# Optimization experiments

Measured on AMD Instinct MI355X. Metric: run time of the kernel, lower is better.

The kernel has to match this reference:

```python
import jax, jax.numpy as jnp
import numpy as np
from jax import lax

RADIUS = 4
SIGMA_1 = 5.0
SIGMA_2 = 1.0


def _gaussian_kernel_3d(radius, sigma):
    x = np.linspace(-radius, radius, 2 * radius + 1)
    xx, yy, zz = np.meshgrid(x, x, x)
    dist2 = xx ** 2 + yy ** 2 + zz ** 2
    k = np.exp(-dist2 / (2.0 * sigma ** 2)).astype(np.float32)
    return jnp.asarray(k)[None, None]  # [O=1, I=1, D, H, W]


def _conv3d_same(x, kernel, radius):
    # x: [B,1,D,H,W], kernel: [1,1,kd,kh,kw]
    pad = [(radius, radius)] * 3
    return lax.conv_general_dilated(
        x, kernel, window_strides=(1, 1, 1), padding=pad,
        dimension_numbers=('NCDHW', 'OIDHW', 'NCDHW'))


def setup_inputs() -> dict:
    key = jax.random.key(0)
    k1, k2 = jax.random.split(key)
    labels = jax.random.uniform(k1, (4, 1, 160, 160, 160), dtype=jnp.float32)
    inputs = jax.random.uniform(k2, (4, 1, 160, 160, 160), dtype=jnp.float32)
    return {"labels": labels, "inputs": inputs}


def reference(labels, inputs):
    kernel = _gaussian_kernel_3d(RADIUS, SIGMA_1)
    num_classes = 2
    p0 = labels[:, 0:1]  # [B,1,D,H,W]
    loss = jnp.float32(0.0)
    for k in range(num_classes):
        class_probs = p0 if k == 0 else 1.0 - p0
        class_mean = (jnp.mean(inputs * class_probs, axis=(2, 3, 4), keepdims=True)
                      / (jnp.mean(class_probs, axis=(2, 3, 4), keepdims=True) + 1e-5))
        diff = jnp.sum((inputs - class_mean) ** 2, axis=1, keepdims=True)  # [B,1,D,H,W]
        weights = jnp.exp(-(diff ** 2) / (SIGMA_2 ** 2))
        numerator = jnp.sum(class_probs * _conv3d_same(class_probs * weights, kernel, RADIUS))
        denominator = jnp.sum(class_probs * _conv3d_same(weights, kernel, RADIUS))
        # L1Loss(scalar, 0) == abs(scalar)
        loss = loss + jnp.abs(numerator / (denominator + 1e-6))
    return jnp.float32(num_classes) - loss
```

## Files before the change

kernel.cpp:

```cpp
#include <hip/hip_runtime.h>
#include <math.h>

#define NX   160
#define N2   25600
#define N3   4096000
#define NB   4
#define TILE 32
#define HALO 4
#define LW   40

#define NTILES_XY 16000
#define TILES_PER_B 4000
#define NBLK_Z 800

__device__ __constant__ float G1[9] = {
    0.72614903f, 0.83527021f, 0.92311635f, 0.98019867f, 1.0f,
    0.98019867f, 0.92311635f, 0.83527021f, 0.72614903f};

__device__ inline float edge_sum(int i) {
    float s = 0.f;
#pragma unroll
    for (int d = 0; d < 9; ++d) {
        int j = i + d - 4;
        s += (j >= 0 && j < NX) ? G1[d] : 0.f;
    }
    return s;
}

template <int NV>
__device__ inline void block_reduce_store(double* vals, double* dst) {
    __shared__ double red[4][NV];
    int lane = threadIdx.x & 63;
    int wave = threadIdx.x >> 6;
#pragma unroll
    for (int v = 0; v < NV; ++v) {
        double x = vals[v];
#pragma unroll
        for (int off = 32; off > 0; off >>= 1) x += __shfl_down(x, off, 64);
        if (lane == 0) red[wave][v] = x;
    }
    __syncthreads();
    if (threadIdx.x < NV) {
        int v = threadIdx.x;
        dst[v] = red[0][v] + red[1][v] + red[2][v] + red[3][v];
    }
}

__global__ __launch_bounds__(256) void conv_xy_kernel(
    const float* __restrict__ labels, const float* __restrict__ inputs,
    float* __restrict__ t, double* __restrict__ pS) {
    __shared__ float sA[LW][LW];
    __shared__ float sB[LW][TILE + 1];

    int bid = blockIdx.x;
    int tileX = bid % 5;
    int tileY = (bid / 5) % 5;
    int zb = bid / 25;
    int sliceOff = zb * N2;
    int x0 = tileX * TILE, y0 = tileY * TILE;
    int tid = threadIdx.x;

    for (int i = tid; i < LW * LW; i += 256) {
        int ly = i / LW, lx = i % LW;
        int gx = x0 + lx - HALO, gy = y0 + ly - HALO;
        float v = 0.f;
        if (gx >= 0 && gx < NX && gy >= 0 && gy < NX)
            v = labels[sliceOff + gy * NX + gx];
        sA[ly][lx] = v;
    }
    __syncthreads();

    for (int i = tid; i < LW * TILE; i += 256) {
        int ly = i / TILE, ox = i % TILE;
        float s = 0.f;
#pragma unroll
        for (int d = 0; d < 9; ++d) s += G1[d] * sA[ly][ox + d];
        sB[ly][ox] = s;
    }
    __syncthreads();

    double lp = 0.0, lip = 0.0, li = 0.0;
    for (int i = tid; i < TILE * TILE; i += 256) {
        int oy = i / TILE, ox = i % TILE;
        float s = 0.f;
#pragma unroll
        for (int d = 0; d < 9; ++d) s += G1[d] * sB[oy + d][ox];
        int gi = sliceOff + (y0 + oy) * NX + (x0 + ox);
        t[gi] = s;
        float p = sA[oy + HALO][ox + HALO];
        float in = inputs[gi];
        lp += (double)p;
        lip += (double)in * (double)p;
        li += (double)in;
    }
    double vals[3] = {lp, lip, li};
    block_reduce_store<3>(vals, pS + 3 * bid);
}

__global__ __launch_bounds__(256) void reduce_S_kernel(
    const double* __restrict__ pS, double* __restrict__ S) {
    int b = blockIdx.x;
    double v0 = 0, v1 = 0, v2 = 0;
    for (int i = threadIdx.x; i < TILES_PER_B; i += 256) {
        const double* p = pS + 3 * (b * TILES_PER_B + i);
        v0 += p[0]; v1 += p[1]; v2 += p[2];
    }
    double vals[3] = {v0, v1, v2};
    block_reduce_store<3>(vals, S + 3 * b);
}

__device__ inline float4 f4_axpy(float a, float4 b, float4 c) {
    return make_float4(c.x + a * b.x, c.y + a * b.y, c.z + a * b.z, c.w + a * b.w);
}

__global__ __launch_bounds__(256) void conv_z_reduce_kernel(
    const float* __restrict__ t, const float* __restrict__ labels,
    const float* __restrict__ inputs, const double* __restrict__ S,
    double* __restrict__ pZ) {
    int tidg = blockIdx.x * 256 + threadIdx.x;
    int x4 = tidg % 40;
    int r = tidg / 40;
    int y = r % NX;
    r /= NX;
    int zc = r % 8;
    int b = r / 8;

    double sp = S[3 * b + 0], sip = S[3 * b + 1], si = S[3 * b + 2];
    const double Nv = (double)N3;
    float m0 = (float)((sip / Nv) / (sp / Nv + 1e-5));
    float m1 = (float)(((si - sip) / Nv) / ((Nv - sp) / Nv + 1e-5));

    int x = x4 * 4;
    float ey = edge_sum(y);
    float4 Cxy = make_float4(edge_sum(x) * ey, edge_sum(x + 1) * ey,
                             edge_sum(x + 2) * ey, edge_sum(x + 3) * ey);

    int z0 = zc * 20;
    int base = b * N3 + y * NX + x;

    float4 win[9];
#pragma unroll
    for (int d = 0; d < 9; ++d) {
        int z = z0 - 4 + d;
        win[d] = (z >= 0 && z < NX) ? *(const float4*)&t[base + z * N2]
                                    : make_float4(0.f, 0.f, 0.f, 0.f);
    }

    double n0 = 0, d0 = 0, n1 = 0, d1 = 0;
    for (int z = z0; z < z0 + 20; ++z) {
        float4 c = make_float4(0.f, 0.f, 0.f, 0.f);
#pragma unroll
        for (int d = 0; d < 9; ++d) c = f4_axpy(G1[d], win[d], c);
        int gi = base + z * N2;
        float4 p = *(const float4*)&labels[gi];
        float4 in = *(const float4*)&inputs[gi];
        float ez = edge_sum(z);
        float pc[4] = {p.x, p.y, p.z, p.w};
        float ic[4] = {in.x, in.y, in.z, in.w};
        float cc[4] = {c.x, c.y, c.z, c.w};
        float cx[4] = {Cxy.x, Cxy.y, Cxy.z, Cxy.w};
#pragma unroll
        for (int j = 0; j < 4; ++j) {
            float c1 = cx[j] * ez - cc[j];
            float df0 = ic[j] - m0; df0 *= df0;
            float w0 = __expf(-df0 * df0);
            float df1 = ic[j] - m1; df1 *= df1;
            float w1 = __expf(-df1 * df1);
            n0 += (double)(cc[j] * pc[j] * w0);
            d0 += (double)(cc[j] * w0);
            n1 += (double)(c1 * (1.f - pc[j]) * w1);
            d1 += (double)(c1 * w1);
        }
#pragma unroll
        for (int d = 0; d < 8; ++d) win[d] = win[d + 1];
        int zn = z + 5;
        win[8] = (zn < NX) ? *(const float4*)&t[base + zn * N2]
                           : make_float4(0.f, 0.f, 0.f, 0.f);
    }
    double vals[4] = {n0, d0, n1, d1};
    block_reduce_store<4>(vals, pZ + 4 * blockIdx.x);
}

__global__ __launch_bounds__(256) void finalize_kernel(
    const double* __restrict__ pZ, float* __restrict__ out) {
    double a0 = 0, a1 = 0, a2 = 0, a3 = 0;
    for (int i = threadIdx.x; i < NBLK_Z; i += 256) {
        const double* p = pZ + 4 * i;
        a0 += p[0]; a1 += p[1]; a2 += p[2]; a3 += p[3];
    }
    double vals[4] = {a0, a1, a2, a3};
    __shared__ double acc[4];
    {
        __shared__ double red[4][4];
        int lane = threadIdx.x & 63;
        int wave = threadIdx.x >> 6;
#pragma unroll
        for (int v = 0; v < 4; ++v) {
            double x = vals[v];
#pragma unroll
            for (int off = 32; off > 0; off >>= 1) x += __shfl_down(x, off, 64);
            if (lane == 0) red[wave][v] = x;
        }
        __syncthreads();
        if (threadIdx.x < 4) {
            int v = threadIdx.x;
            acc[v] = red[0][v] + red[1][v] + red[2][v] + red[3][v];
        }
        __syncthreads();
    }
    if (threadIdx.x == 0) {
        double r0 = fabs(acc[0] / (acc[1] + 1e-6));
        double r1 = fabs(acc[2] / (acc[3] + 1e-6));
        out[0] = (float)(2.0 - r0 - r1);
    }
}

extern "C" void kernel_launch(void* const* d_in, const int* in_sizes, int n_in,
                              void* d_out, int out_size, void* d_ws, size_t ws_size,
                              hipStream_t stream) {
    const float* labels = (const float*)d_in[0];
    const float* inputs = (const float*)d_in[1];
    float* out = (float*)d_out;

    double* pS = (double*)d_ws;
    double* S  = (double*)((char*)d_ws + 384000);
    double* pZ = (double*)((char*)d_ws + 384096);
    float*  t  = (float*)((char*)d_ws + 524288);

    hipLaunchKernelGGL(conv_xy_kernel, dim3(NTILES_XY), dim3(256), 0, stream,
                       labels, inputs, t, pS);
    hipLaunchKernelGGL(reduce_S_kernel, dim3(NB), dim3(256), 0, stream, pS, S);
    hipLaunchKernelGGL(conv_z_reduce_kernel, dim3(NBLK_Z), dim3(256), 0, stream,
                       t, labels, inputs, S, pZ);
    hipLaunchKernelGGL(finalize_kernel, dim3(1), dim3(256), 0, stream, pZ, out);
}
```

Measured before the change: 236.9 us.

## Vectorize xy conv with float4, batch z loads, use float accumulators

The xy convolution now loads halo tiles and writes output with float4 accesses. Each thread computes four outputs per row with register-held windows, and each thread produces one float4 output, so the stride loop is gone. The z-pass kernel batches four z-slices of loads ahead of compute to raise memory-level parallelism and accumulates in float instead of double. edge_sum becomes a closed-form lookup, and finalize is simplified. Float accumulation over 20×16 terms per thread risks some precision loss, and the wider loads raise register pressure.

```diff
diff --git a/kernel.cpp b/kernel.cpp
--- a/kernel.cpp
+++ b/kernel.cpp
@@ -5,26 +5,31 @@
 #define N2   25600
 #define N3   4096000
 #define NB   4
-#define TILE 32
-#define HALO 4
-#define LW   40
 
 #define NTILES_XY 16000
 #define TILES_PER_B 4000
 #define NBLK_Z 800
 
+#define SA_W 52
+#define SB_W 36
+
 __device__ __constant__ float G1[9] = {
     0.72614903f, 0.83527021f, 0.92311635f, 0.98019867f, 1.0f,
     0.98019867f, 0.92311635f, 0.83527021f, 0.72614903f};
 
+#define ES_FULL 7.92946852f
+__device__ __constant__ float ES_M[4] = {3.46473426f, 2.48453559f, 1.56141924f,
+                                         0.72614903f};
 __device__ inline float edge_sum(int i) {
-    float s = 0.f;
-#pragma unroll
-    for (int d = 0; d < 9; ++d) {
-        int j = i + d - 4;
-        s += (j >= 0 && j < NX) ? G1[d] : 0.f;
-    }
+    float s = ES_FULL;
+    if (i < 4) s -= ES_M[i];
+    if (i > NX - 5) s -= ES_M[NX - 1 - i];
     return s;
+}
+
+__device__ inline float4 f4_zero() { return make_float4(0.f, 0.f, 0.f, 0.f); }
+__device__ inline float4 f4_axpy(float a, float4 b, float4 c) {
+    return make_float4(c.x + a * b.x, c.y + a * b.y, c.z + a * b.z, c.w + a * b.w);
 }
 
 template <int NV>
@@ -49,51 +54,65 @@
 __global__ __launch_bounds__(256) void conv_xy_kernel(
     const float* __restrict__ labels, const float* __restrict__ inputs,
     float* __restrict__ t, double* __restrict__ pS) {
-    __shared__ float sA[LW][LW];
-    __shared__ float sB[LW][TILE + 1];
+    __shared__ float sA[40 * SA_W];
+    __shared__ float sB[40 * SB_W];
 
     int bid = blockIdx.x;
     int tileX = bid % 5;
     int tileY = (bid / 5) % 5;
     int zb = bid / 25;
     int sliceOff = zb * N2;
-    int x0 = tileX * TILE, y0 = tileY * TILE;
+    int x0 = tileX * 32, y0 = tileY * 32;
     int tid = threadIdx.x;
 
-    for (int i = tid; i < LW * LW; i += 256) {
-        int ly = i / LW, lx = i % LW;
-        int gx = x0 + lx - HALO, gy = y0 + ly - HALO;
-        float v = 0.f;
-        if (gx >= 0 && gx < NX && gy >= 0 && gy < NX)
-            v = labels[sliceOff + gy * NX + gx];
-        sA[ly][lx] = v;
-    }
-    __syncthreads();
-
-    for (int i = tid; i < LW * TILE; i += 256) {
-        int ly = i / TILE, ox = i % TILE;
-        float s = 0.f;
-#pragma unroll
-        for (int d = 0; d < 9; ++d) s += G1[d] * sA[ly][ox + d];
-        sB[ly][ox] = s;
-    }
-    __syncthreads();
-
-    double lp = 0.0, lip = 0.0, li = 0.0;
-    for (int i = tid; i < TILE * TILE; i += 256) {
-        int oy = i / TILE, ox = i % TILE;
-        float s = 0.f;
-#pragma unroll
-        for (int d = 0; d < 9; ++d) s += G1[d] * sB[oy + d][ox];
-        int gi = sliceOff + (y0 + oy) * NX + (x0 + ox);
-        t[gi] = s;
-        float p = sA[oy + HALO][ox + HALO];
-        float in = inputs[gi];
-        lp += (double)p;
-        lip += (double)in * (double)p;
-        li += (double)in;
-    }
-    double vals[3] = {lp, lip, li};
+    for (int i = tid; i < 480; i += 256) {
+        int row = i / 12, c = i % 12;
+        int gx = x0 - 8 + 4 * c;
+        int gy = y0 - 4 + row;
+        float4 v = f4_zero();
+        if (gy >= 0 && gy < NX && gx >= 0 && gx <= NX - 4)
+            v = *(const float4*)&labels[sliceOff + gy * NX + gx];
+        *(float4*)&sA[row * SA_W + 4 * c] = v;
+    }
+    __syncthreads();
+
+    for (int i = tid; i < 320; i += 256) {
+        int r = i >> 3, x4 = i & 7;
+        const float* row = &sA[r * SA_W + 4 * x4];
+        float4 a = *(const float4*)&row[4];
+        float4 b = *(const float4*)&row[8];
+        float4 c = *(const float4*)&row[12];
+        float w[12] = {a.x, a.y, a.z, a.w, b.x, b.y, b.z, b.w,
+                       c.x, c.y, c.z, c.w};
+        float4 o = f4_zero();
+#pragma unroll
+        for (int d = 0; d < 9; ++d) {
+            float g = G1[d];
+            o.x += g * w[d];
+            o.y += g * w[d + 1];
+            o.z += g * w[d + 2];
+            o.w += g * w[d + 3];
+        }
+        *(float4*)&sB[r * SB_W + 4 * x4] = o;
+    }
+    __syncthreads();
+
+    int oy = tid >> 3, x4 = tid & 7;
+    float4 acc = f4_zero();
+#pragma unroll
+    for (int d = 0; d < 9; ++d) {
+        float4 v = *(const float4*)&sB[(oy + d) * SB_W + 4 * x4];
+        acc = f4_axpy(G1[d], v, acc);
+    }
+    int gi = sliceOff + (y0 + oy) * NX + (x0 + 4 * x4);
+    *(float4*)&t[gi] = acc;
+
+    float4 p = *(const float4*)&sA[(oy + 4) * SA_W + 4 * x4 + 8];
+    float4 in = *(const float4*)&inputs[gi];
+    float sp = p.x + p.y + p.z + p.w;
+    float sip = in.x * p.x + in.y * p.y + in.z * p.z + in.w * p.w;
+    float si = in.x + in.y + in.z + in.w;
+    double vals[3] = {(double)sp, (double)sip, (double)si};
     block_reduce_store<3>(vals, pS + 3 * bid);
 }
 
@@ -107,10 +126,6 @@
     }
     double vals[3] = {v0, v1, v2};
     block_reduce_store<3>(vals, S + 3 * b);
-}
-
-__device__ inline float4 f4_axpy(float a, float4 b, float4 c) {
-    return make_float4(c.x + a * b.x, c.y + a * b.y, c.z + a * b.z, c.w + a * b.w);
 }
 
 __global__ __launch_bounds__(256) void conv_z_reduce_kernel(
@@ -132,8 +147,8 @@
 
     int x = x4 * 4;
     float ey = edge_sum(y);
-    float4 Cxy = make_float4(edge_sum(x) * ey, edge_sum(x + 1) * ey,
-                             edge_sum(x + 2) * ey, edge_sum(x + 3) * ey);
+    float cx[4] = {edge_sum(x) * ey, edge_sum(x + 1) * ey,
+                   edge_sum(x + 2) * ey, edge_sum(x + 3) * ey};
 
     int z0 = zc * 20;
     int base = b * N3 + y * NX + x;
@@ -143,41 +158,48 @@
     for (int d = 0; d < 9; ++d) {
         int z = z0 - 4 + d;
         win[d] = (z >= 0 && z < NX) ? *(const float4*)&t[base + z * N2]
-                                    : make_float4(0.f, 0.f, 0.f, 0.f);
-    }
-
-    double n0 = 0, d0 = 0, n1 = 0, d1 = 0;
-    for (int z = z0; z < z0 + 20; ++z) {
-        float4 c = make_float4(0.f, 0.f, 0.f, 0.f);
-#pragma unroll
-        for (int d = 0; d < 9; ++d) c = f4_axpy(G1[d], win[d], c);
-        int gi = base + z * N2;
-        float4 p = *(const float4*)&labels[gi];
-        float4 in = *(const float4*)&inputs[gi];
-        float ez = edge_sum(z);
-        float pc[4] = {p.x, p.y, p.z, p.w};
-        float ic[4] = {in.x, in.y, in.z, in.w};
-        float cc[4] = {c.x, c.y, c.z, c.w};
-        float cx[4] = {Cxy.x, Cxy.y, Cxy.z, Cxy.w};
+                                    : f4_zero();
+    }
+
+    float n0 = 0.f, d0 = 0.f, n1 = 0.f, d1 = 0.f;
+    for (int zb = 0; zb < 5; ++zb) {
+        int z = z0 + 4 * zb;
+        float4 tn[4], pv[4], iv[4];
 #pragma unroll
         for (int j = 0; j < 4; ++j) {
-            float c1 = cx[j] * ez - cc[j];
-            float df0 = ic[j] - m0; df0 *= df0;
-            float w0 = __expf(-df0 * df0);
-            float df1 = ic[j] - m1; df1 *= df1;
-            float w1 = __expf(-df1 * df1);
-            n0 += (double)(cc[j] * pc[j] * w0);
-            d0 += (double)(cc[j] * w0);
-            n1 += (double)(c1 * (1.f - pc[j]) * w1);
-            d1 += (double)(c1 * w1);
+            int zl = z + j + 5;
+            tn[j] = (zl < NX) ? *(const float4*)&t[base + zl * N2] : f4_zero();
+            int gi = base + (z + j) * N2;
+            pv[j] = *(const float4*)&labels[gi];
+            iv[j] = *(const float4*)&inputs[gi];
         }
 #pragma unroll
-        for (int d = 0; d < 8; ++d) win[d] = win[d + 1];
-        int zn = z + 5;
-        win[8] = (zn < NX) ? *(const float4*)&t[base + zn * N2]
-                           : make_float4(0.f, 0.f, 0.f, 0.f);
-    }
-    double vals[4] = {n0, d0, n1, d1};
+        for (int j = 0; j < 4; ++j) {
+            float4 c4 = f4_zero();
+#pragma unroll
+            for (int d = 0; d < 9; ++d) c4 = f4_axpy(G1[d], win[d], c4);
+            float ez = edge_sum(z + j);
+            float pc[4] = {pv[j].x, pv[j].y, pv[j].z, pv[j].w};
+            float ic[4] = {iv[j].x, iv[j].y, iv[j].z, iv[j].w};
+            float cc[4] = {c4.x, c4.y, c4.z, c4.w};
+#pragma unroll
+            for (int l = 0; l < 4; ++l) {
+                float c1 = cx[l] * ez - cc[l];
+                float df0 = ic[l] - m0; df0 *= df0;
+                float w0 = __expf(-df0 * df0);
+                float df1 = ic[l] - m1; df1 *= df1;
+                float w1 = __expf(-df1 * df1);
+                n0 += cc[l] * pc[l] * w0;
+                d0 += cc[l] * w0;
+                n1 += c1 * (1.f - pc[l]) * w1;
+                d1 += c1 * w1;
+            }
+#pragma unroll
+            for (int d = 0; d < 8; ++d) win[d] = win[d + 1];
+            win[8] = tn[j];
+        }
+    }
+    double vals[4] = {(double)n0, (double)d0, (double)n1, (double)d1};
     block_reduce_store<4>(vals, pZ + 4 * blockIdx.x);
 }
 
@@ -188,27 +210,23 @@
         const double* p = pZ + 4 * i;
         a0 += p[0]; a1 += p[1]; a2 += p[2]; a3 += p[3];
     }
+    __shared__ double red[4][4];
+    int lane = threadIdx.x & 63;
+    int wave = threadIdx.x >> 6;
     double vals[4] = {a0, a1, a2, a3};
-    __shared__ double acc[4];
-    {
-        __shared__ double red[4][4];
-        int lane = threadIdx.x & 63;
-        int wave = threadIdx.x >> 6;
-#pragma unroll
-        for (int v = 0; v < 4; ++v) {
-            double x = vals[v];
-#pragma unroll
-            for (int off = 32; off > 0; off >>= 1) x += __shfl_down(x, off, 64);
-            if (lane == 0) red[wave][v] = x;
-        }
-        __syncthreads();
-        if (threadIdx.x < 4) {
-            int v = threadIdx.x;
+#pragma unroll
+    for (int v = 0; v < 4; ++v) {
+        double x = vals[v];
+#pragma unroll
+        for (int off = 32; off > 0; off >>= 1) x += __shfl_down(x, off, 64);
+        if (lane == 0) red[wave][v] = x;
+    }
+    __syncthreads();
+    if (threadIdx.x == 0) {
+        double acc[4];
+#pragma unroll
+        for (int v = 0; v < 4; ++v)
             acc[v] = red[0][v] + red[1][v] + red[2][v] + red[3][v];
-        }
-        __syncthreads();
-    }
-    if (threadIdx.x == 0) {
         double r0 = fabs(acc[0] / (acc[1] + 1e-6));
         double r1 = fabs(acc[2] / (acc[3] + 1e-6));
         out[0] = (float)(2.0 - r0 - r1);
```

Result: faster. 206.4 us (-12.9%).
